# Kernel tuning notes

Hardware: AMD Instinct MI355X
Metric: run time of the kernel (lower is better)

Reference implementation:

```python
import jax, jax.numpy as jnp
import numpy as np

B, L, H = 8, 1024, 1024
E, K, I = 8, 2, 256
N_SHARED = 2
IS = I * N_SHARED
NHEADS = 4
HD = H // NHEADS
EPS = 1e-6


def rmsnorm(x, w):
    xf = x.astype(jnp.float32)
    var = jnp.mean(xf * xf, axis=-1, keepdims=True)
    return w * (xf * jax.lax.rsqrt(var + EPS)).astype(x.dtype)


def setup_inputs():
    key = jax.random.key(0)
    ks = jax.random.split(key, 12)
    s = 0.02
    return {
        "hidden_states": jax.random.normal(ks[0], (B, L, H), jnp.float32),
        "true_counts": jax.random.randint(ks[1], (B,), 1, L + 1),
        "context_norm_w": jnp.ones((H,), jnp.float32),
        "in_proj_w": jax.random.normal(ks[2], (3 * H, H), jnp.float32) * s,
        "in_proj_b": jnp.zeros((3 * H,), jnp.float32),
        "out_proj_w": jax.random.normal(ks[3], (H, H), jnp.float32) * s,
        "out_proj_b": jnp.zeros((H,), jnp.float32),
        "gate_norm_w": jnp.ones((H,), jnp.float32),
        "gate_w": jax.random.normal(ks[4], (E, H), jnp.float32) * s,
        "expert_norm_w": jnp.ones((E, H), jnp.float32),
        "expert_gate_w": jax.random.normal(ks[5], (E, I, H), jnp.float32) * s,
        "expert_up_w": jax.random.normal(ks[6], (E, I, H), jnp.float32) * s,
        "expert_down_w": jax.random.normal(ks[7], (E, H, I), jnp.float32) * s,
        "shared_norm_w": jnp.ones((H,), jnp.float32),
        "shared_gate_w": jax.random.normal(ks[8], (IS, H), jnp.float32) * s,
        "shared_up_w": jax.random.normal(ks[9], (IS, H), jnp.float32) * s,
        "shared_down_w": jax.random.normal(ks[10], (H, IS), jnp.float32) * s,
        "out_gate_w": jnp.zeros((1, H), jnp.float32),
        "out_gate_b": jnp.zeros((1,), jnp.float32),
    }


def reference(hidden_states, true_counts, context_norm_w, in_proj_w, in_proj_b,
              out_proj_w, out_proj_b, gate_norm_w, gate_w, expert_norm_w,
              expert_gate_w, expert_up_w, expert_down_w, shared_norm_w,
              shared_gate_w, shared_up_w, shared_down_w, out_gate_w, out_gate_b):
    Bq, Lq, Hq = hidden_states.shape
    pad = jnp.arange(Lq)[None, :] >= true_counts[:, None]  # [B,L] True = padding

    # --- pre-norm self-attention context layer (eval mode: no dropout) ---
    nx = rmsnorm(hidden_states, context_norm_w)
    qkv = nx @ in_proj_w.T + in_proj_b
    q, k, v = jnp.split(qkv, 3, axis=-1)
    def heads(t):
        return t.reshape(Bq, Lq, NHEADS, HD).transpose(0, 2, 1, 3)
    q, k, v = heads(q), heads(k), heads(v)
    att = jnp.einsum('bhqd,bhkd->bhqk', q, k) / np.float32(np.sqrt(HD))
    att = jnp.where(pad[:, None, None, :], jnp.finfo(att.dtype).min, att)
    att = jax.nn.softmax(att, axis=-1)
    ctx = jnp.einsum('bhqk,bhkd->bhqd', att, v).transpose(0, 2, 1, 3).reshape(Bq, Lq, Hq)
    ctx = ctx @ out_proj_w.T + out_proj_b
    x = hidden_states + ctx
    identity = x

    xf = x.reshape(-1, Hq)  # [N,H]
    N = xf.shape[0]

    # --- top-k gating ---
    gscores = jax.nn.softmax(rmsnorm(xf, gate_norm_w) @ gate_w.T, axis=-1)  # [N,E]
    topw, topi = jax.lax.top_k(gscores, K)
    topw = topw / (jnp.sum(topw, axis=-1, keepdims=True) + 1e-20)  # norm_topk_prob
    w_ne = jnp.zeros((N, E), xf.dtype).at[jnp.arange(N)[:, None], topi].set(topw)

    # --- routed experts: each expert has its own RMSNorm; fold the norm weight
    # into the gate/up projections since rms scale of x is expert-independent ---
    xf32 = xf.astype(jnp.float32)
    xhat = xf * jax.lax.rsqrt(jnp.mean(xf32 * xf32, axis=-1, keepdims=True) + EPS)
    wg = expert_gate_w * expert_norm_w[:, None, :]  # [E,I,H]
    wu = expert_up_w * expert_norm_w[:, None, :]
    g = jax.nn.silu(jnp.einsum('nh,eih->nei', xhat, wg))
    u = jnp.einsum('nh,eih->nei', xhat, wu)
    # weighted combine folded into the down projection (linear in the intermediate)
    y = jnp.einsum('nei,ne,ehi->nh', g * u, w_ne, expert_down_w)
    y = y.reshape(Bq, Lq, Hq)

    # --- shared experts ---
    sx = rmsnorm(identity, shared_norm_w)
    y = y + (jax.nn.silu(sx @ shared_gate_w.T) * (sx @ shared_up_w.T)) @ shared_down_w.T

    # --- output gate + padding mask ---
    gate_score = jax.nn.sigmoid(y @ out_gate_w.T + out_gate_b)  # [B,L,1]
    y_gated = y * gate_score
    y_gated = jnp.where(pad[..., None], jnp.zeros((), y.dtype), y_gated)
    return y_gated
```

## Files before the change

kernel.cpp:

```cpp
#include <hip/hip_runtime.h>
#include <hip/hip_bf16.h>

typedef unsigned short u16;
typedef unsigned int   u32;
typedef short bf16x8 __attribute__((ext_vector_type(8)));
typedef float f32x4  __attribute__((ext_vector_type(4)));

#define DEV static __device__ __forceinline__

#define Bc 8
#define Lc 1024
#define Hc 1024
#define Ec 8
#define Ic 256
#define ISc 512
#define NHc 4
#define HDc 256
#define NTOK 8192
#define EPSc 1e-6f
#define MAXSLOTS 17408

DEV u16 f2bf(float f){
  u32 u = __float_as_uint(f);
  return (u16)((u + 0x7fffu + ((u >> 16) & 1u)) >> 16);
}
DEV float bf2f(u16 h){ return __uint_as_float(((u32)h) << 16); }

DEV void gload_lds16(const void* g, void* l){
  __builtin_amdgcn_global_load_lds((const __attribute__((address_space(1))) u32*)g,
                                   (__attribute__((address_space(3))) u32*)l, 16, 0, 0);
}

DEV bool compact_m0(const int* __restrict__ tc, int slot, int& m0){
  int cb[8], Lt = 0;
#pragma unroll
  for (int b = 0; b < 8; b++){ cb[b] = (tc[b] + 127) >> 7; Lt += cb[b]; }
  const int i = (slot & 7) + 8*(slot >> 3);
  if (i >= Lt) return false;
  int acc = 0, bsel = 0, pos = 0;
#pragma unroll
  for (int b = 0; b < 8; b++){
    if (i < acc + cb[b]){ bsel = b; pos = i - acc; break; }
    acc += cb[b];
  }
  m0 = (bsel*8 + pos)*128;
  return true;
}

template<int EPI, int BIAS, int SKIP, int SWZ, int ZDEC>
__global__ __launch_bounds__(256)
void gemm3(const u16* __restrict__ Ahi, const u16* __restrict__ Alo,
           const u16* __restrict__ Bhi, const u16* __restrict__ Blo,
           void* __restrict__ Cv, const float* __restrict__ bias,
           const float* __restrict__ Res,
           int M, int N, int K, int lda, int ldb, int ldc,
           long sAin, long sAout, long sBin, long sBout, long sCin, long sCout,
           int loOffC, int biasStride, const int* __restrict__ tc, int bbase)
{
  __shared__ u16 lsAh[128*32];
  __shared__ u16 lsAl[128*32];
  __shared__ u16 lsBh[128*32];
  __shared__ u16 lsBl[128*32];
  int m_i, n_i, z;
  if (SWZ == 1){
    const int NB = gridDim.x*gridDim.y;
    const int L = blockIdx.x + gridDim.x*(blockIdx.y + gridDim.y*blockIdx.z);
    const int r = L & 7, k = L >> 3;
    z = r + 8*(k / NB);
    const int idx = k % NB;
    n_i = idx % gridDim.x; m_i = idx / gridDim.x;
  } else if (SWZ == 2){
    m_i = blockIdx.x; n_i = blockIdx.y; z = blockIdx.z;
  } else {
    n_i = blockIdx.x; m_i = blockIdx.y; z = blockIdx.z;
  }
  int n0 = n_i*128, m0 = m_i*128;
  const int zin  = ZDEC ? (z & 7)  : (z & 3);
  const int zout = ZDEC ? (z >> 3) : (z >> 2);
  if (SKIP == 1){ const int c = tc[bbase + zin]; if (m0 >= c || n0 >= c) return; }
  if (SKIP == 2){ const int c = tc[bbase + zin]; if (m0 >= c) return;
                  const int kl = (c + 31) & ~31; K = K < kl ? K : kl; }
  if (SKIP == 3){ if ((m0 & 1023) >= tc[m0 >> 10]) return; }
  if (SKIP == 4){ if (!compact_m0(tc, m_i, m0)) return; }
  const long aoff = (long)zin*sAin + (long)zout*sAout;
  const long boff = (long)zin*sBin + (long)zout*sBout;
  const long coff = (long)zin*sCin + (long)zout*sCout;
  const u16* Ahb = Ahi + aoff;
  const u16* Alb = Alo + aoff;
  const u16* Bhb = Bhi + boff;
  const u16* Blb = Blo + boff;
  const int t = threadIdx.x, lane = t & 63;
  const int w = t >> 6, wm = w >> 1, wn = w & 1;
  const int fr = lane & 15, kg = lane >> 4;
  const int srow = t >> 2, scol = (t & 3) * 8;
  f32x4 acc[4][4] = {};

  for (int kb = 0; kb < K; kb += 32){
    gload_lds16(Ahb + (long)(m0 +      srow)*lda + kb + scol, &lsAh[srow*32 + scol]);
    gload_lds16(Ahb + (long)(m0 + 64 + srow)*lda + kb + scol, &lsAh[(64+srow)*32 + scol]);
    gload_lds16(Alb + (long)(m0 +      srow)*lda + kb + scol, &lsAl[srow*32 + scol]);
    gload_lds16(Alb + (long)(m0 + 64 + srow)*lda + kb + scol, &lsAl[(64+srow)*32 + scol]);
    gload_lds16(Bhb + (long)(n0 +      srow)*ldb + kb + scol, &lsBh[srow*32 + scol]);
    gload_lds16(Bhb + (long)(n0 + 64 + srow)*ldb + kb + scol, &lsBh[(64+srow)*32 + scol]);
    gload_lds16(Blb + (long)(n0 +      srow)*ldb + kb + scol, &lsBl[srow*32 + scol]);
    gload_lds16(Blb + (long)(n0 + 64 + srow)*ldb + kb + scol, &lsBl[(64+srow)*32 + scol]);
    asm volatile("s_waitcnt vmcnt(0)" ::: "memory");
    __syncthreads();
    bf16x8 ah[4], al[4], bh[4], bl[4];
#pragma unroll
    for (int i = 0; i < 4; i++){
      ah[i] = *(const bf16x8*)&lsAh[(wm*64 + i*16 + fr)*32 + kg*8];
      al[i] = *(const bf16x8*)&lsAl[(wm*64 + i*16 + fr)*32 + kg*8];
      bh[i] = *(const bf16x8*)&lsBh[(wn*64 + i*16 + fr)*32 + kg*8];
      bl[i] = *(const bf16x8*)&lsBl[(wn*64 + i*16 + fr)*32 + kg*8];
    }
#pragma unroll
    for (int mi = 0; mi < 4; mi++)
#pragma unroll
      for (int ni = 0; ni < 4; ni++){
        acc[mi][ni] = __builtin_amdgcn_mfma_f32_16x16x32_bf16(ah[mi], bh[ni], acc[mi][ni], 0, 0, 0);
        acc[mi][ni] = __builtin_amdgcn_mfma_f32_16x16x32_bf16(ah[mi], bl[ni], acc[mi][ni], 0, 0, 0);
        acc[mi][ni] = __builtin_amdgcn_mfma_f32_16x16x32_bf16(al[mi], bh[ni], acc[mi][ni], 0, 0, 0);
      }
    __syncthreads();
  }

  const int r4 = (lane >> 4) * 4;
#pragma unroll
  for (int mi = 0; mi < 4; mi++){
#pragma unroll
    for (int ni = 0; ni < 4; ni++){
      const int col = n0 + wn*64 + ni*16 + fr;
      const float bb = BIAS ? bias[zin*biasStride + col] : 0.f;
#pragma unroll
      for (int r = 0; r < 4; r++){
        const int row = m0 + wm*64 + mi*16 + r4 + r;
        float v = acc[mi][ni][r] + bb;
        if (EPI == 0){
          u16 hv = f2bf(v), lv = f2bf(v - bf2f(hv));
          long idx = coff + (long)row*ldc + col;
          ((u16*)Cv)[idx] = hv;
          ((u16*)Cv)[idx + loOffC] = lv;
        } else if (EPI == 1){
          ((float*)Cv)[coff + (long)row*ldc + col] = v;
        } else if (EPI == 2){
          long idx = coff + (long)row*ldc + col;
          ((float*)Cv)[idx] = v + Res[idx];
        } else if (EPI == 3){
          u16 hv = f2bf(v), lv = f2bf(v - bf2f(hv));
          int b = row >> 10, q = row & 1023;
          int h = col >> 8, d = col & 255;
          long o = ((long)(b*NHc + h)*HDc + d)*2048 + q;
          ((u16*)Cv)[o] = hv;
          ((u16*)Cv)[o + 1024] = lv;
        } else {
          u16 hv = f2bf(v), lv = f2bf(v - bf2f(hv));
          if (z < 2){
            long idx = (long)z*sCin + (long)row*ldc + col;
            ((u16*)Cv)[idx] = hv;
            ((u16*)Cv)[idx + loOffC] = lv;
          } else {
            int b = row >> 10, q = row & 1023;
            int h = col >> 8, d = col & 255;
            long o = sCout + ((long)(b*NHc + h)*HDc + d)*2048 + q;
            ((u16*)Cv)[o] = hv;
            ((u16*)Cv)[o + 1024] = lv;
          }
        }
      }
    }
  }
}

template<int EPI, int SKIP, int SWZ>
__global__ __launch_bounds__(256)
void gemm_bt(const u16* __restrict__ A, const u16* __restrict__ B,
             void* __restrict__ Cv,
             int M, int N, int K, int lda, int ldb, int ldc,
             long sAz, long sBz, long sCz, const int* __restrict__ tc)
{
  __shared__ u16 lsA[128*32];
  __shared__ u16 lsB[128*32];
  int m_i, n_i;
  if (SWZ == 2){ m_i = blockIdx.x; n_i = blockIdx.y; }
  else         { n_i = blockIdx.x; m_i = blockIdx.y; }
  const int z = blockIdx.z;
  int n0 = n_i*128, m0 = m_i*128;
  if (SKIP == 3){ if ((m0 & 1023) >= tc[m0 >> 10]) return; }
  if (SKIP == 4){ if (!compact_m0(tc, m_i, m0)) return; }
  const u16* Ab = A + (long)z*sAz;
  const u16* Bb = B + (long)z*sBz;
  const int t = threadIdx.x, lane = t & 63;
  const int w = t >> 6, wm = w >> 1, wn = w & 1;
  const int fr = lane & 15, kg = lane >> 4;
  const int srow = t >> 2, scol = (t & 3) * 8;
  f32x4 acc[4][4] = {};

  for (int kb = 0; kb < K; kb += 32){
    gload_lds16(Ab + (long)(m0 +      srow)*lda + kb + scol, &lsA[srow*32 + scol]);
    gload_lds16(Ab + (long)(m0 + 64 + srow)*lda + kb + scol, &lsA[(64+srow)*32 + scol]);
    gload_lds16(Bb + (long)(n0 +      srow)*ldb + kb + scol, &lsB[srow*32 + scol]);
    gload_lds16(Bb + (long)(n0 + 64 + srow)*ldb + kb + scol, &lsB[(64+srow)*32 + scol]);
    asm volatile("s_waitcnt vmcnt(0)" ::: "memory");
    __syncthreads();
    bf16x8 av[4], bv[4];
#pragma unroll
    for (int i = 0; i < 4; i++){
      av[i] = *(const bf16x8*)&lsA[(wm*64 + i*16 + fr)*32 + kg*8];
      bv[i] = *(const bf16x8*)&lsB[(wn*64 + i*16 + fr)*32 + kg*8];
    }
#pragma unroll
    for (int mi = 0; mi < 4; mi++)
#pragma unroll
      for (int ni = 0; ni < 4; ni++)
        acc[mi][ni] = __builtin_amdgcn_mfma_f32_16x16x32_bf16(av[mi], bv[ni], acc[mi][ni], 0, 0, 0);
    __syncthreads();
  }

  const int r4 = (lane >> 4) * 4;
#pragma unroll
  for (int mi = 0; mi < 4; mi++){
#pragma unroll
    for (int ni = 0; ni < 4; ni++){
      const int col = n0 + wn*64 + ni*16 + fr;
#pragma unroll
      for (int r = 0; r < 4; r++){
        const int row = m0 + wm*64 + mi*16 + r4 + r;
        const long idx = (long)z*sCz + (long)row*ldc + col;
        float v = acc[mi][ni][r];
        if      (EPI == 0) ((u16*)Cv)[idx]   = f2bf(v);
        else if (EPI == 1) ((float*)Cv)[idx] = v;
        else               ((float*)Cv)[idx] += v;
      }
    }
  }
}

__global__ __launch_bounds__(256)
void gemm_gu_gather(const u16* __restrict__ A, const u16* __restrict__ Ball,
                    u16* __restrict__ Cg, const int* __restrict__ sidx,
                    const int* __restrict__ counts, const int* __restrict__ offs)
{
  __shared__ u16 lsA[128*32];
  __shared__ u16 lsB[128*32];
  const int e = blockIdx.z;
  const int cnt = counts[e];
  const int obase = offs[e];
  const int padc = offs[e+1] - obase;
  const int m0 = blockIdx.y*128;
  if (m0 >= padc) return;
  const int n0 = blockIdx.x*128;
  const u16* B = Ball + (long)e*512*1024;
  const int t = threadIdx.x, lane = t & 63;
  const int w = t >> 6, wm = w >> 1, wn = w & 1;
  const int fr = lane & 15, kg = lane >> 4;
  const int srow = t >> 2, scol = (t & 3) * 8;
  const int s0 = m0 + srow, s1 = m0 + 64 + srow;
  const int tok0 = (s0 < cnt) ? sidx[e*NTOK + s0] : 0;
  const int tok1 = (s1 < cnt) ? sidx[e*NTOK + s1] : 0;
  f32x4 acc[4][4] = {};

  for (int kb = 0; kb < 1024; kb += 32){
    gload_lds16(A + (long)tok0*1024 + kb + scol, &lsA[srow*32 + scol]);
    gload_lds16(A + (long)tok1*1024 + kb + scol, &lsA[(64+srow)*32 + scol]);
    gload_lds16(B + (long)(n0 +      srow)*1024 + kb + scol, &lsB[srow*32 + scol]);
    gload_lds16(B + (long)(n0 + 64 + srow)*1024 + kb + scol, &lsB[(64+srow)*32 + scol]);
    asm volatile("s_waitcnt vmcnt(0)" ::: "memory");
    __syncthreads();
    bf16x8 av[4], bv[4];
#pragma unroll
    for (int i = 0; i < 4; i++){
      av[i] = *(const bf16x8*)&lsA[(wm*64 + i*16 + fr)*32 + kg*8];
      bv[i] = *(const bf16x8*)&lsB[(wn*64 + i*16 + fr)*32 + kg*8];
    }
#pragma unroll
    for (int mi = 0; mi < 4; mi++)
#pragma unroll
      for (int ni = 0; ni < 4; ni++)
        acc[mi][ni] = __builtin_amdgcn_mfma_f32_16x16x32_bf16(av[mi], bv[ni], acc[mi][ni], 0, 0, 0);
    __syncthreads();
  }

  const int r4 = (lane >> 4) * 4;
#pragma unroll
  for (int mi = 0; mi < 4; mi++){
#pragma unroll
    for (int ni = 0; ni < 4; ni++){
      const int col = wn*64 + ni*16 + fr + n0;
#pragma unroll
      for (int r = 0; r < 4; r++){
        const int row = m0 + wm*64 + mi*16 + r4 + r;
        Cg[(long)(obase + row)*512 + col] = f2bf(acc[mi][ni][r]);
      }
    }
  }
}

__global__ __launch_bounds__(256)
void gemm_down_slots(const u16* __restrict__ Zg, const u16* __restrict__ Wd,
                     u16* __restrict__ D, const int* __restrict__ offs)
{
  __shared__ u16 lsA[128*32];
  __shared__ u16 lsB[128*32];
  const int m0 = blockIdx.y*128;
  if (m0 >= offs[8]) return;
  int e = 0;
#pragma unroll
  for (int i = 0; i < 7; i++) if (m0 >= offs[i+1]) e = i+1;
  const u16* B = Wd + (long)e*1024*256;
  const int n0 = blockIdx.x*128;
  const int t = threadIdx.x, lane = t & 63;
  const int w = t >> 6, wm = w >> 1, wn = w & 1;
  const int fr = lane & 15, kg = lane >> 4;
  const int srow = t >> 2, scol = (t & 3) * 8;
  f32x4 acc[4][4] = {};

  for (int kb = 0; kb < 256; kb += 32){
    gload_lds16(Zg + (long)(m0 +      srow)*256 + kb + scol, &lsA[srow*32 + scol]);
    gload_lds16(Zg + (long)(m0 + 64 + srow)*256 + kb + scol, &lsA[(64+srow)*32 + scol]);
    gload_lds16(B  + (long)(n0 +      srow)*256 + kb + scol, &lsB[srow*32 + scol]);
    gload_lds16(B  + (long)(n0 + 64 + srow)*256 + kb + scol, &lsB[(64+srow)*32 + scol]);
    asm volatile("s_waitcnt vmcnt(0)" ::: "memory");
    __syncthreads();
    bf16x8 av[4], bv[4];
#pragma unroll
    for (int i = 0; i < 4; i++){
      av[i] = *(const bf16x8*)&lsA[(wm*64 + i*16 + fr)*32 + kg*8];
      bv[i] = *(const bf16x8*)&lsB[(wn*64 + i*16 + fr)*32 + kg*8];
    }
#pragma unroll
    for (int mi = 0; mi < 4; mi++)
#pragma unroll
      for (int ni = 0; ni < 4; ni++)
        acc[mi][ni] = __builtin_amdgcn_mfma_f32_16x16x32_bf16(av[mi], bv[ni], acc[mi][ni], 0, 0, 0);
    __syncthreads();
  }

  const int r4 = (lane >> 4) * 4;
#pragma unroll
  for (int mi = 0; mi < 4; mi++){
#pragma unroll
    for (int ni = 0; ni < 4; ni++){
      const int col = n0 + wn*64 + ni*16 + fr;
#pragma unroll
      for (int r = 0; r < 4; r++){
        const int row = m0 + wm*64 + mi*16 + r4 + r;
        D[(long)row*1024 + col] = f2bf(acc[mi][ni][r]);
      }
    }
  }
}

__global__ void cast_bf16_k(const float* __restrict__ in, u16* __restrict__ out, long n){
  long i = (long)blockIdx.x*blockDim.x + threadIdx.x;
  long st = (long)gridDim.x*blockDim.x;
  for (; i < n; i += st) out[i] = f2bf(in[i]);
}

__global__ void split_cast_k(const float* __restrict__ in, u16* __restrict__ hi,
                             u16* __restrict__ lo, long n){
  long i = (long)blockIdx.x*blockDim.x + threadIdx.x;
  long st = (long)gridDim.x*blockDim.x;
  for (; i < n; i += st){
    float v = in[i];
    u16 h = f2bf(v);
    hi[i] = h;
    lo[i] = f2bf(v - bf2f(h));
  }
}

__global__ void fold_expert_k(const float* __restrict__ g, const float* __restrict__ u,
                              const float* __restrict__ nw, u16* __restrict__ gu, long n){
  long i = (long)blockIdx.x*blockDim.x + threadIdx.x;
  long st = (long)gridDim.x*blockDim.x;
  for (; i < n; i += st){
    int h  = (int)(i & (Hc - 1));
    int ii = (int)((i >> 10) & (Ic - 1));
    int e  = (int)(i >> 18);
    float wv = nw[e*Hc + h];
    long o = (long)e*(2*Ic*Hc) + (long)ii*Hc + h;
    gu[o]         = f2bf(g[i]*wv);
    gu[o + Ic*Hc] = f2bf(u[i]*wv);
  }
}

__global__ __launch_bounds__(256)
void rmsnorm_split_k(const float* __restrict__ x, const float* __restrict__ w1,
                     u16* __restrict__ o){
  const int row = blockIdx.x, t = threadIdx.x, lane = t & 63, w = t >> 6;
  float4 v = ((const float4*)(x + (long)row*Hc))[t];
  float ss = v.x*v.x + v.y*v.y + v.z*v.z + v.w*v.w;
  for (int off = 32; off; off >>= 1) ss += __shfl_xor(ss, off);
  __shared__ float red[4];
  if (lane == 0) red[w] = ss;
  __syncthreads();
  float rs = rsqrtf((red[0]+red[1]+red[2]+red[3])*(1.f/Hc) + EPSc);
  float4 wv = ((const float4*)w1)[t];
  float f0 = v.x*rs*wv.x, f1 = v.y*rs*wv.y, f2 = v.z*rs*wv.z, f3 = v.w*rs*wv.w;
  ushort4 hv, lv;
  hv.x = f2bf(f0); lv.x = f2bf(f0 - bf2f(hv.x));
  hv.y = f2bf(f1); lv.y = f2bf(f1 - bf2f(hv.y));
  hv.z = f2bf(f2); lv.z = f2bf(f2 - bf2f(hv.z));
  hv.w = f2bf(f3); lv.w = f2bf(f3 - bf2f(hv.w));
  u16* r16 = o + (long)row*2048;
  ((ushort4*)r16)[t] = hv;
  ((ushort4*)(r16 + 1024))[t] = lv;
}

__global__ __launch_bounds__(256)
void norm_gate_k(const float* __restrict__ x, const float* __restrict__ shw,
                 const float* __restrict__ gnw, const float* __restrict__ gw,
                 const int* __restrict__ tcnt,
                 u16* __restrict__ xhat, u16* __restrict__ sx,
                 int* __restrict__ topi, float* __restrict__ topw){
  const int row = blockIdx.x, t = threadIdx.x, lane = t & 63, w = t >> 6;
  float4 v = ((const float4*)(x + (long)row*Hc))[t];
  float ss = v.x*v.x + v.y*v.y + v.z*v.z + v.w*v.w;
  for (int off = 32; off; off >>= 1) ss += __shfl_xor(ss, off);
  __shared__ float red[4];
  __shared__ float gred[4][8];
  if (lane == 0) red[w] = ss;
  __syncthreads();
  float rs = rsqrtf((red[0]+red[1]+red[2]+red[3])*(1.f/Hc) + EPSc);
  ushort4 ov;
  ov.x = f2bf(v.x*rs); ov.y = f2bf(v.y*rs); ov.z = f2bf(v.z*rs); ov.w = f2bf(v.w*rs);
  ((ushort4*)xhat)[(long)row*256 + t] = ov;
  float4 sv = ((const float4*)shw)[t];
  ov.x = f2bf(v.x*rs*sv.x); ov.y = f2bf(v.y*rs*sv.y);
  ov.z = f2bf(v.z*rs*sv.z); ov.w = f2bf(v.w*rs*sv.w);
  ((ushort4*)sx)[(long)row*256 + t] = ov;

  const int b = row >> 10, l = row & 1023;
  if (l >= tcnt[b]) return;
  float4 g = ((const float4*)gnw)[t];
  float xg0 = v.x*g.x, xg1 = v.y*g.y, xg2 = v.z*g.z, xg3 = v.w*g.w;
  float pe[8];
#pragma unroll
  for (int e = 0; e < 8; e++){
    float4 ww = ((const float4*)(gw + (long)e*Hc))[t];
    pe[e] = xg0*ww.x + xg1*ww.y + xg2*ww.z + xg3*ww.w;
  }
  for (int off = 32; off; off >>= 1){
#pragma unroll
    for (int e = 0; e < 8; e++) pe[e] += __shfl_xor(pe[e], off);
  }
  if (lane == 0){
#pragma unroll
    for (int e = 0; e < 8; e++) gred[w][e] = pe[e];
  }
  __syncthreads();
  if (t == 0){
    float sc[8], m = -3.4e38f;
#pragma unroll
    for (int e = 0; e < 8; e++){
      sc[e] = (gred[0][e]+gred[1][e]+gred[2][e]+gred[3][e])*rs;
      m = fmaxf(m, sc[e]);
    }
    float p[8], sum = 0.f;
#pragma unroll
    for (int e = 0; e < 8; e++){ p[e] = __expf(sc[e] - m); sum += p[e]; }
    float inv = 1.f/sum;
#pragma unroll
    for (int e = 0; e < 8; e++) p[e] *= inv;
    int i1 = 0; float v1 = p[0];
#pragma unroll
    for (int e = 1; e < 8; e++) if (p[e] > v1){ v1 = p[e]; i1 = e; }
    int i2 = -1; float v2 = -1.f;
#pragma unroll
    for (int e = 0; e < 8; e++) if (e != i1 && p[e] > v2){ v2 = p[e]; i2 = e; }
    float dn = v1 + v2 + 1e-20f;
    topi[2*row] = i1; topi[2*row + 1] = i2;
    topw[2*row] = v1/dn; topw[2*row + 1] = v2/dn;
  }
}

__global__ __launch_bounds__(256)
void softmax2_k(float* __restrict__ S, const int* __restrict__ cnt, int bbase, int bmask){
  const int rid = blockIdx.x;
  const int b = bbase + ((rid >> 10) & bmask);
  const int n = cnt[b];
  if ((rid & 1023) >= n) return;
  float* row = S + (long)rid*Lc;
  const int t = threadIdx.x, lane = t & 63, w = t >> 6;
  float4 v = ((const float4*)row)[t];
  const float sc = 0.0625f;
  float vals[4] = {v.x*sc, v.y*sc, v.z*sc, v.w*sc};
  const int c = t*4;
  float m = -3.4e38f;
#pragma unroll
  for (int j = 0; j < 4; j++) if (c + j < n) m = fmaxf(m, vals[j]);
  for (int o = 32; o; o >>= 1) m = fmaxf(m, __shfl_xor(m, o));
  __shared__ float red[8];
  if (lane == 0) red[w] = m;
  __syncthreads();
  m = fmaxf(fmaxf(red[0], red[1]), fmaxf(red[2], red[3]));
  float p[4], s = 0.f;
#pragma unroll
  for (int j = 0; j < 4; j++){ p[j] = (c + j < n) ? __expf(vals[j] - m) : 0.f; s += p[j]; }
  for (int o = 32; o; o >>= 1) s += __shfl_xor(s, o);
  if (lane == 0) red[4 + w] = s;
  __syncthreads();
  const float inv = 1.f / (red[4]+red[5]+red[6]+red[7]);
  ushort4 hv, lv;
  float q0 = p[0]*inv, q1 = p[1]*inv, q2 = p[2]*inv, q3 = p[3]*inv;
  hv.x = f2bf(q0); lv.x = f2bf(q0 - bf2f(hv.x));
  hv.y = f2bf(q1); lv.y = f2bf(q1 - bf2f(hv.y));
  hv.z = f2bf(q2); lv.z = f2bf(q2 - bf2f(hv.z));
  hv.w = f2bf(q3); lv.w = f2bf(q3 - bf2f(hv.w));
  u16* r16 = (u16*)S + (long)rid*2048;
  ((ushort4*)r16)[t] = hv;
  ((ushort4*)(r16 + 1024))[t] = lv;
}

__global__ __launch_bounds__(1024)
void route_scan_k(const int* __restrict__ tcnt, const int* __restrict__ topi,
                  const float* __restrict__ topw, int* __restrict__ counts,
                  int* __restrict__ offs, int* __restrict__ sidx,
                  int* __restrict__ gpos, float* __restrict__ wG){
  __shared__ int hist[1024][8];
  __shared__ int soffs[9];
  const int t = threadIdx.x;
  for (int i = t; i < MAXSLOTS; i += 1024) wG[i] = 0.f;
  int h[8] = {0,0,0,0,0,0,0,0};
  const int n0 = t*8;
  int e0[8], e1[8];
#pragma unroll
  for (int k = 0; k < 8; k++){
    const int n = n0 + k;
    const int b = n >> 10, l = n & 1023;
    const bool val = l < tcnt[b];
    e0[k] = val ? topi[2*n]   : -1;
    e1[k] = val ? topi[2*n+1] : -1;
    if (val){ h[e0[k]]++; h[e1[k]]++; }
  }
#pragma unroll
  for (int e = 0; e < 8; e++) hist[t][e] = h[e];
  __syncthreads();
  for (int off = 1; off < 1024; off <<= 1){
    int v[8];
#pragma unroll
    for (int e = 0; e < 8; e++)
      v[e] = hist[t][e] + ((t >= off) ? hist[t - off][e] : 0);
    __syncthreads();
#pragma unroll
    for (int e = 0; e < 8; e++) hist[t][e] = v[e];
    __syncthreads();
  }
  if (t == 0){
    int o = 0; soffs[0] = 0; offs[0] = 0;
    for (int e = 0; e < 8; e++){
      int c = hist[1023][e];
      counts[e] = c;
      o += (c + 127) & ~127;
      soffs[e+1] = o;
      offs[e+1] = o;
    }
  }
  __syncthreads();
  int run[8];
#pragma unroll
  for (int e = 0; e < 8; e++) run[e] = hist[t][e] - h[e];
#pragma unroll
  for (int k = 0; k < 8; k++){
    const int n = n0 + k;
    if (e0[k] >= 0){
      const int p0 = run[e0[k]]++;
      const int p1 = run[e1[k]]++;
      sidx[e0[k]*NTOK + p0] = n;
      sidx[e1[k]*NTOK + p1] = n;
      const int g0 = soffs[e0[k]] + p0, g1 = soffs[e1[k]] + p1;
      gpos[2*n] = g0; gpos[2*n+1] = g1;
      wG[g0] = topw[2*n]; wG[g1] = topw[2*n+1];
    } else {
      gpos[2*n] = 0; gpos[2*n+1] = 0;
    }
  }
}

__global__ void act_shared_k(const u16* __restrict__ gu, u16* __restrict__ z, long n){
  long i = (long)blockIdx.x*blockDim.x + threadIdx.x;
  long st = (long)gridDim.x*blockDim.x;
  for (; i < n; i += st){
    long nn = i >> 9;
    int  ii = (int)(i & (ISc - 1));
    float gv = bf2f(gu[nn*1024 + ii]);
    float uv = bf2f(gu[nn*1024 + ISc + ii]);
    z[i] = f2bf(gv/(1.f + __expf(-gv)) * uv);
  }
}

__global__ void act_slots_k(const u16* __restrict__ gu, const float* __restrict__ wG,
                            const int* __restrict__ offs, u16* __restrict__ z){
  long nmax = (long)offs[8]*256;
  long st = (long)gridDim.x*blockDim.x;
  for (long i = (long)blockIdx.x*blockDim.x + threadIdx.x; i < nmax; i += st){
    long s = i >> 8;
    int ii = (int)(i & 255);
    float gv = bf2f(gu[s*512 + ii]);
    float uv = bf2f(gu[s*512 + 256 + ii]);
    z[i] = f2bf(gv/(1.f + __expf(-gv)) * uv * wG[s]);
  }
}

__global__ void act_expert_k(const u16* __restrict__ gu, const int* __restrict__ topi,
                             const float* __restrict__ topw, int e,
                             u16* __restrict__ z, long n){
  long i = (long)blockIdx.x*blockDim.x + threadIdx.x;
  long st = (long)gridDim.x*blockDim.x;
  for (; i < n; i += st){
    long nn = i >> 8;
    int  ii = (int)(i & (Ic - 1));
    float wv = 0.f;
    if      (topi[2*nn]     == e) wv = topw[2*nn];
    else if (topi[2*nn + 1] == e) wv = topw[2*nn + 1];
    float gv = bf2f(gu[nn*512 + ii]);
    float uv = bf2f(gu[nn*512 + Ic + ii]);
    z[i] = f2bf(gv/(1.f + __expf(-gv)) * uv * wv);
  }
}

__global__ __launch_bounds__(256)
void final2_k(const float* __restrict__ ysh, const u16* __restrict__ D,
              const int* __restrict__ gpos, const float* __restrict__ ogw,
              const float* __restrict__ ogb, const int* __restrict__ cnt,
              float* __restrict__ out){
  const int t = threadIdx.x, lane = t & 63, w = t >> 6;
  const int n = blockIdx.x*4 + w;
  const int b = n >> 10, l = n & 1023;
  float* outr = out + (long)n*Hc;
  if (l >= cnt[b]){
#pragma unroll
    for (int j = 0; j < 16; j++) outr[j*64 + lane] = 0.f;
    return;
  }
  const float* yr = ysh + (long)n*Hc;
  const u16* d0 = D + (long)gpos[2*n]*1024;
  const u16* d1 = D + (long)gpos[2*n+1]*1024;
  float dot = 0.f, yv[16];
#pragma unroll
  for (int j = 0; j < 16; j++){
    int d = j*64 + lane;
    yv[j] = yr[d] + bf2f(d0[d]) + bf2f(d1[d]);
    dot += yv[j]*ogw[d];
  }
  for (int o = 32; o; o >>= 1) dot += __shfl_xor(dot, o);
  float s = 1.f/(1.f + __expf(-(dot + ogb[0])));
#pragma unroll
  for (int j = 0; j < 16; j++) outr[j*64 + lane] = yv[j]*s;
}

__global__ __launch_bounds__(256)
void final_k(const float* __restrict__ y, const float* __restrict__ ogw,
             const float* __restrict__ ogb, const int* __restrict__ cnt,
             float* __restrict__ out){
  const int t = threadIdx.x, lane = t & 63, w = t >> 6;
  const int n = blockIdx.x*4 + w;
  const int b = n >> 10, l = n & 1023;
  const bool pad = l >= cnt[b];
  const float* yr = y + (long)n*Hc;
  float dot = 0.f, yv[16];
#pragma unroll
  for (int j = 0; j < 16; j++){
    int d = j*64 + lane;
    yv[j] = yr[d];
    dot += yv[j]*ogw[d];
  }
  for (int o = 32; o; o >>= 1) dot += __shfl_xor(dot, o);
  float s = 1.f/(1.f + __expf(-(dot + ogb[0])));
  float* outr = out + (long)n*Hc;
#pragma unroll
  for (int j = 0; j < 16; j++){
    int d = j*64 + lane;
    outr[d] = pad ? 0.f : yv[j]*s;
  }
}

__global__ void sentinel_k(float* out){ out[0] = 1.0e9f; }

extern "C" void kernel_launch(void* const* d_in, const int* in_sizes, int n_in,
                              void* d_out, int out_size, void* d_ws, size_t ws_size,
                              hipStream_t stream){
  const float* hidden  = (const float*)d_in[0];
  const int*   cnt     = (const int*)  d_in[1];
  const float* ctx_nw  = (const float*)d_in[2];
  const float* Wqkv    = (const float*)d_in[3];
  const float* in_b    = (const float*)d_in[4];
  const float* Woutp   = (const float*)d_in[5];
  const float* out_b   = (const float*)d_in[6];
  const float* gate_nw = (const float*)d_in[7];
  const float* gate_w  = (const float*)d_in[8];
  const float* exp_nw  = (const float*)d_in[9];
  const float* Weg     = (const float*)d_in[10];
  const float* Weu     = (const float*)d_in[11];
  const float* Wed     = (const float*)d_in[12];
  const float* sh_nw   = (const float*)d_in[13];
  const float* Wsg     = (const float*)d_in[14];
  const float* Wsu     = (const float*)d_in[15];
  const float* Wsd     = (const float*)d_in[16];
  const float* ogw     = (const float*)d_in[17];
  const float* ogb     = (const float*)d_in[18];
  float* out = (float*)d_out;

  const size_t MB = 1024*1024;
  char* ws = (char*)d_ws;
  size_t off = 0;
  auto alloc = [&](size_t bytes)->char*{
    char* p = ws + off; off += (bytes + 255) & ~(size_t)255; return p;
  };
  u16* wWqH  = (u16*)alloc((size_t)3072*1024*2);
  u16* wWqL  = (u16*)alloc((size_t)3072*1024*2);
  u16* wWoH  = (u16*)alloc((size_t)1024*1024*2);
  u16* wWoL  = (u16*)alloc((size_t)1024*1024*2);
  u16* wWgu  = (u16*)alloc((size_t)Ec*2*Ic*Hc*2);
  u16* wWd   = (u16*)alloc((size_t)Ec*Hc*Ic*2);
  u16* wWsgu = (u16*)alloc((size_t)2*ISc*Hc*2);
  u16* wWsd  = (u16*)alloc((size_t)Hc*ISc*2);
  int*   wTopI = (int*)  alloc((size_t)NTOK*2*4);
  float* wTopW = (float*)alloc((size_t)NTOK*2*4);
  int*   wGpos = (int*)  alloc((size_t)NTOK*2*4);
  int*   wSidx = (int*)  alloc((size_t)Ec*NTOK*4);
  float* wG    = (float*)alloc((size_t)MAXSLOTS*4);
  int*   wCnts = (int*)  alloc(64);
  int*   wOffs = (int*)  alloc(64);
  char* P1 = alloc(32*MB);
  char* P2 = alloc(32*MB);
  char* P3 = alloc(32*MB);
  char* P4 = alloc(32*MB);
  size_t fixed = off;
  const int mode = (fixed + 128*MB <= ws_size) ? 2 :
                   (fixed + 64*MB  <= ws_size) ? 1 : 0;
  char* P5 = alloc(mode == 2 ? 128*MB : mode == 1 ? 64*MB : 16*MB);
  if (off > ws_size){ sentinel_k<<<1,1,0,stream>>>(out); return; }

  u16*   wNx   = (u16*)P1;
  u16*   wCtx  = (u16*)P1;
  float* wY    = (float*)P1;
  u16*   wQp   = (u16*)P2;
  u16*   wXhat = (u16*)P2;
  u16*   wSx   = (u16*)(P2 + 16*MB);
  u16*   wKp   = (u16*)P3;
  float* wX    = (float*)P3;
  u16*   wGUg  = (u16*)P3;
  u16*   wZg   = (u16*)(P3 + 18*MB);
  u16*   wGUe  = (u16*)P3;
  u16*   wZe   = (u16*)(P3 + 8*MB);
  u16*   wVtp  = (u16*)P4;
  u16*   wGUs  = (u16*)P4;
  u16*   wZs   = (u16*)(P4 + 16*MB);
  float* wS    = (float*)P5;
  u16*   wD    = (u16*)P5;

  split_cast_k<<<4096, 256, 0, stream>>>(Wqkv,  wWqH, wWqL, (long)3072*1024);
  split_cast_k<<<2048, 256, 0, stream>>>(Woutp, wWoH, wWoL, (long)1024*1024);
  cast_bf16_k<<<2048, 256, 0, stream>>>(Wed, wWd, (long)Ec*Hc*Ic);
  cast_bf16_k<<<1024, 256, 0, stream>>>(Wsg, wWsgu,                (long)ISc*Hc);
  cast_bf16_k<<<1024, 256, 0, stream>>>(Wsu, wWsgu + (long)ISc*Hc, (long)ISc*Hc);
  cast_bf16_k<<<1024, 256, 0, stream>>>(Wsd, wWsd, (long)Hc*ISc);
  fold_expert_k<<<2048, 256, 0, stream>>>(Weg, Weu, exp_nw, wWgu, (long)Ec*Ic*Hc);

  rmsnorm_split_k<<<NTOK, 256, 0, stream>>>(hidden, ctx_nw, wNx);
  gemm3<4, 1, 4, 2, 0><<<dim3(64, 8, 3), 256, 0, stream>>>(
      wNx, wNx + 1024, wWqH, wWqL, wQp, in_b, nullptr,
      NTOK, 1024, 1024, 2048, 1024, 2048,
      0, 0, (long)1024*1024, 0,
      (long)16*1024*1024,
      (long)32*1024*1024,
      1024, 1024, cnt, 0);

  if (mode == 2){
    gemm3<1, 0, 1, 1, 1><<<dim3(8, 8, 32), 256, 0, stream>>>(
        wQp, wQp + 1024, wKp, wKp + 1024, wS, nullptr, nullptr,
        Lc, Lc, HDc, 2048, 2048, Lc,
        (long)Lc*2048, (long)HDc,
        (long)Lc*2048, (long)HDc,
        (long)Lc*Lc,   (long)8*Lc*Lc,
        0, 0, cnt, 0);
    softmax2_k<<<32*1024, 256, 0, stream>>>(wS, cnt, 0, 7);
    gemm3<0, 0, 2, 1, 1><<<dim3(2, 8, 32), 256, 0, stream>>>(
        (const u16*)wS, (const u16*)wS + 1024, wVtp, wVtp + 1024, wCtx,
        nullptr, nullptr,
        Lc, HDc, Lc, 2048, 2048, 2048,
        (long)Lc*2048,      (long)8*Lc*2048,
        (long)NHc*HDc*2048, (long)HDc*2048,
        (long)Lc*2048,      (long)HDc,
        1024, 0, cnt, 0);
  } else if (mode == 1){
    for (int g = 0; g < 2; g++){
      const int bbase = g*4;
      const long tokoff = (long)g*4*Lc*2048;
      const u16* Qb = wQp + tokoff;
      const u16* Kb = wKp + tokoff;
      gemm3<1, 0, 1, 1, 0><<<dim3(8, 8, 16), 256, 0, stream>>>(
          Qb, Qb + 1024, Kb, Kb + 1024, wS, nullptr, nullptr,
          Lc, Lc, HDc, 2048, 2048, Lc,
          (long)Lc*2048, (long)HDc,
          (long)Lc*2048, (long)HDc,
          (long)Lc*Lc,   (long)4*Lc*Lc,
          0, 0, cnt, bbase);
      softmax2_k<<<16*1024, 256, 0, stream>>>(wS, cnt, bbase, 3);
      const u16* Vb = wVtp + (long)g*4*NHc*HDc*2048;
      u16* Cb = wCtx + tokoff;
      gemm3<0, 0, 2, 1, 0><<<dim3(2, 8, 16), 256, 0, stream>>>(
          (const u16*)wS, (const u16*)wS + 1024, Vb, Vb + 1024, Cb, nullptr, nullptr,
          Lc, HDc, Lc, 2048, 2048, 2048,
          (long)Lc*2048,     (long)4*Lc*2048,
          (long)NHc*HDc*2048,(long)HDc*2048,
          (long)Lc*2048,     (long)HDc,
          1024, 0, cnt, bbase);
    }
  } else {
    for (int g = 0; g < 8; g++){
      const int hf = g >> 2, hbase = g & 3, bbase = hf*4;
      const long tokoff = (long)hf*4*Lc*2048;
      const u16* Qb = wQp + tokoff + hbase*HDc;
      const u16* Kb = wKp + tokoff + hbase*HDc;
      gemm3<1, 0, 1, 0, 0><<<dim3(8, 8, 4), 256, 0, stream>>>(
          Qb, Qb + 1024, Kb, Kb + 1024, wS, nullptr, nullptr,
          Lc, Lc, HDc, 2048, 2048, Lc,
          (long)Lc*2048, (long)HDc,
          (long)Lc*2048, (long)HDc,
          (long)Lc*Lc,   (long)4*Lc*Lc,
          0, 0, cnt, bbase);
      softmax2_k<<<4*1024, 256, 0, stream>>>(wS, cnt, bbase, 3);
      const u16* Vb = wVtp + (long)hf*4*NHc*HDc*2048 + (long)hbase*HDc*2048;
      u16* Cb = wCtx + tokoff + hbase*HDc;
      gemm3<0, 0, 2, 0, 0><<<dim3(2, 8, 4), 256, 0, stream>>>(
          (const u16*)wS, (const u16*)wS + 1024, Vb, Vb + 1024, Cb, nullptr, nullptr,
          Lc, HDc, Lc, 2048, 2048, 2048,
          (long)Lc*2048,     (long)4*Lc*2048,
          (long)NHc*HDc*2048,(long)HDc*2048,
          (long)Lc*2048,     (long)HDc,
          1024, 0, cnt, bbase);
    }
  }

  gemm3<2, 1, 4, 2, 0><<<dim3(64, 8, 1), 256, 0, stream>>>(
      wCtx, wCtx + 1024, wWoH, wWoL, wX, out_b, hidden,
      NTOK, 1024, 1024, 2048, 1024, 1024,
      0, 0, 0, 0, 0, 0, 0, 0, cnt, 0);

  norm_gate_k<<<NTOK, 256, 0, stream>>>(wX, sh_nw, gate_nw, gate_w, cnt,
                                        wXhat, wSx, wTopI, wTopW);
  route_scan_k<<<1, 1024, 0, stream>>>(cnt, wTopI, wTopW, wCnts, wOffs,
                                       wSidx, wGpos, wG);

  gemm_bt<0, 4, 2><<<dim3(64, 8, 1), 256, 0, stream>>>(
      wSx, wWsgu, wGUs, NTOK, 2*ISc, 1024, 1024, 1024, 2*ISc, 0, 0, 0, cnt);
  act_shared_k<<<4096, 256, 0, stream>>>(wGUs, wZs, (long)NTOK*ISc);
  gemm_bt<1, 4, 2><<<dim3(64, 8, 1), 256, 0, stream>>>(
      wZs, wWsd, wY, NTOK, 1024, ISc, ISc, ISc, 1024, 0, 0, 0, cnt);

  if (mode >= 1){
    gemm_gu_gather<<<dim3(4, 64, Ec), 256, 0, stream>>>(
        wXhat, wWgu, wGUg, wSidx, wCnts, wOffs);
    act_slots_k<<<2048, 256, 0, stream>>>(wGUg, wG, wOffs, wZg);
    gemm_down_slots<<<dim3(8, MAXSLOTS/128, 1), 256, 0, stream>>>(
        wZg, wWd, wD, wOffs);
    final2_k<<<NTOK/4, 256, 0, stream>>>(wY, wD, wGpos, ogw, ogb, cnt, out);
  } else {
    for (int e = 0; e < Ec; e++){
      gemm_bt<0, 0, 0><<<dim3(4, 64, 1), 256, 0, stream>>>(
          wXhat, wWgu + (long)e*2*Ic*Hc, wGUe, NTOK, 2*Ic, 1024, 1024, 1024, 2*Ic,
          0, 0, 0, nullptr);
      act_expert_k<<<2048, 256, 0, stream>>>(wGUe, wTopI, wTopW, e, wZe, (long)NTOK*Ic);
      gemm_bt<2, 0, 0><<<dim3(8, 64, 1), 256, 0, stream>>>(
          wZe, wWd + (long)e*Hc*Ic, wY, NTOK, 1024, Ic, Ic, Ic, 1024, 0, 0, 0, nullptr);
    }
    final_k<<<NTOK/4, 256, 0, stream>>>(wY, ogw, ogb, cnt, out);
  }
}
```

Baseline: 661.9 us.

## Double-buffer LDS tiles in all MFMA GEMM kernels to overlap loads with compute

Converts the four GEMM kernels (split-precision gemm3, gemm_bt, the gathered expert gate/up GEMM, and the slot-based down GEMM) to use two LDS buffers. Each iteration prefetches the next K-tile while MFMAs run on the current one, hiding global-load latency behind compute. This doubles LDS use per block, to 64 KB for gemm3, which can lower occupancy. It also drops the explicit s_waitcnt vmcnt(0) before the barrier, so correctness relies on __syncthreads waiting for the direct-to-LDS loads to finish.

```diff
diff --git a/kernel.cpp b/kernel.cpp
--- a/kernel.cpp
+++ b/kernel.cpp
@@ -57,10 +57,10 @@
            long sAin, long sAout, long sBin, long sBout, long sCin, long sCout,
            int loOffC, int biasStride, const int* __restrict__ tc, int bbase)
 {
-  __shared__ u16 lsAh[128*32];
-  __shared__ u16 lsAl[128*32];
-  __shared__ u16 lsBh[128*32];
-  __shared__ u16 lsBl[128*32];
+  __shared__ u16 lsAh[2][128*32];
+  __shared__ u16 lsAl[2][128*32];
+  __shared__ u16 lsBh[2][128*32];
+  __shared__ u16 lsBl[2][128*32];
   int m_i, n_i, z;
   if (SWZ == 1){
     const int NB = gridDim.x*gridDim.y;
@@ -95,24 +95,29 @@
   const int srow = t >> 2, scol = (t & 3) * 8;
   f32x4 acc[4][4] = {};
 
+  auto stage = [&](int buf, int kb){
+    gload_lds16(Ahb + (long)(m0 +      srow)*lda + kb + scol, &lsAh[buf][srow*32 + scol]);
+    gload_lds16(Ahb + (long)(m0 + 64 + srow)*lda + kb + scol, &lsAh[buf][(64+srow)*32 + scol]);
+    gload_lds16(Alb + (long)(m0 +      srow)*lda + kb + scol, &lsAl[buf][srow*32 + scol]);
+    gload_lds16(Alb + (long)(m0 + 64 + srow)*lda + kb + scol, &lsAl[buf][(64+srow)*32 + scol]);
+    gload_lds16(Bhb + (long)(n0 +      srow)*ldb + kb + scol, &lsBh[buf][srow*32 + scol]);
+    gload_lds16(Bhb + (long)(n0 + 64 + srow)*ldb + kb + scol, &lsBh[buf][(64+srow)*32 + scol]);
+    gload_lds16(Blb + (long)(n0 +      srow)*ldb + kb + scol, &lsBl[buf][srow*32 + scol]);
+    gload_lds16(Blb + (long)(n0 + 64 + srow)*ldb + kb + scol, &lsBl[buf][(64+srow)*32 + scol]);
+  };
+
+  stage(0, 0);
+  __syncthreads();
+  int cur = 0;
   for (int kb = 0; kb < K; kb += 32){
-    gload_lds16(Ahb + (long)(m0 +      srow)*lda + kb + scol, &lsAh[srow*32 + scol]);
-    gload_lds16(Ahb + (long)(m0 + 64 + srow)*lda + kb + scol, &lsAh[(64+srow)*32 + scol]);
-    gload_lds16(Alb + (long)(m0 +      srow)*lda + kb + scol, &lsAl[srow*32 + scol]);
-    gload_lds16(Alb + (long)(m0 + 64 + srow)*lda + kb + scol, &lsAl[(64+srow)*32 + scol]);
-    gload_lds16(Bhb + (long)(n0 +      srow)*ldb + kb + scol, &lsBh[srow*32 + scol]);
-    gload_lds16(Bhb + (long)(n0 + 64 + srow)*ldb + kb + scol, &lsBh[(64+srow)*32 + scol]);
-    gload_lds16(Blb + (long)(n0 +      srow)*ldb + kb + scol, &lsBl[srow*32 + scol]);
-    gload_lds16(Blb + (long)(n0 + 64 + srow)*ldb + kb + scol, &lsBl[(64+srow)*32 + scol]);
-    asm volatile("s_waitcnt vmcnt(0)" ::: "memory");
-    __syncthreads();
+    if (kb + 32 < K) stage(cur ^ 1, kb + 32);
     bf16x8 ah[4], al[4], bh[4], bl[4];
 #pragma unroll
     for (int i = 0; i < 4; i++){
-      ah[i] = *(const bf16x8*)&lsAh[(wm*64 + i*16 + fr)*32 + kg*8];
-      al[i] = *(const bf16x8*)&lsAl[(wm*64 + i*16 + fr)*32 + kg*8];
-      bh[i] = *(const bf16x8*)&lsBh[(wn*64 + i*16 + fr)*32 + kg*8];
-      bl[i] = *(const bf16x8*)&lsBl[(wn*64 + i*16 + fr)*32 + kg*8];
+      ah[i] = *(const bf16x8*)&lsAh[cur][(wm*64 + i*16 + fr)*32 + kg*8];
+      al[i] = *(const bf16x8*)&lsAl[cur][(wm*64 + i*16 + fr)*32 + kg*8];
+      bh[i] = *(const bf16x8*)&lsBh[cur][(wn*64 + i*16 + fr)*32 + kg*8];
+      bl[i] = *(const bf16x8*)&lsBl[cur][(wn*64 + i*16 + fr)*32 + kg*8];
     }
 #pragma unroll
     for (int mi = 0; mi < 4; mi++)
@@ -123,6 +128,7 @@
         acc[mi][ni] = __builtin_amdgcn_mfma_f32_16x16x32_bf16(al[mi], bh[ni], acc[mi][ni], 0, 0, 0);
       }
     __syncthreads();
+    cur ^= 1;
   }
 
   const int r4 = (lane >> 4) * 4;
@@ -179,8 +185,8 @@
              int M, int N, int K, int lda, int ldb, int ldc,
              long sAz, long sBz, long sCz, const int* __restrict__ tc)
 {
-  __shared__ u16 lsA[128*32];
-  __shared__ u16 lsB[128*32];
+  __shared__ u16 lsA[2][128*32];
+  __shared__ u16 lsB[2][128*32];
   int m_i, n_i;
   if (SWZ == 2){ m_i = blockIdx.x; n_i = blockIdx.y; }
   else         { n_i = blockIdx.x; m_i = blockIdx.y; }
@@ -196,18 +202,23 @@
   const int srow = t >> 2, scol = (t & 3) * 8;
   f32x4 acc[4][4] = {};
 
+  auto stage = [&](int buf, int kb){
+    gload_lds16(Ab + (long)(m0 +      srow)*lda + kb + scol, &lsA[buf][srow*32 + scol]);
+    gload_lds16(Ab + (long)(m0 + 64 + srow)*lda + kb + scol, &lsA[buf][(64+srow)*32 + scol]);
+    gload_lds16(Bb + (long)(n0 +      srow)*ldb + kb + scol, &lsB[buf][srow*32 + scol]);
+    gload_lds16(Bb + (long)(n0 + 64 + srow)*ldb + kb + scol, &lsB[buf][(64+srow)*32 + scol]);
+  };
+
+  stage(0, 0);
+  __syncthreads();
+  int cur = 0;
   for (int kb = 0; kb < K; kb += 32){
-    gload_lds16(Ab + (long)(m0 +      srow)*lda + kb + scol, &lsA[srow*32 + scol]);
-    gload_lds16(Ab + (long)(m0 + 64 + srow)*lda + kb + scol, &lsA[(64+srow)*32 + scol]);
-    gload_lds16(Bb + (long)(n0 +      srow)*ldb + kb + scol, &lsB[srow*32 + scol]);
-    gload_lds16(Bb + (long)(n0 + 64 + srow)*ldb + kb + scol, &lsB[(64+srow)*32 + scol]);
-    asm volatile("s_waitcnt vmcnt(0)" ::: "memory");
-    __syncthreads();
+    if (kb + 32 < K) stage(cur ^ 1, kb + 32);
     bf16x8 av[4], bv[4];
 #pragma unroll
     for (int i = 0; i < 4; i++){
-      av[i] = *(const bf16x8*)&lsA[(wm*64 + i*16 + fr)*32 + kg*8];
-      bv[i] = *(const bf16x8*)&lsB[(wn*64 + i*16 + fr)*32 + kg*8];
+      av[i] = *(const bf16x8*)&lsA[cur][(wm*64 + i*16 + fr)*32 + kg*8];
+      bv[i] = *(const bf16x8*)&lsB[cur][(wn*64 + i*16 + fr)*32 + kg*8];
     }
 #pragma unroll
     for (int mi = 0; mi < 4; mi++)
@@ -215,6 +226,7 @@
       for (int ni = 0; ni < 4; ni++)
         acc[mi][ni] = __builtin_amdgcn_mfma_f32_16x16x32_bf16(av[mi], bv[ni], acc[mi][ni], 0, 0, 0);
     __syncthreads();
+    cur ^= 1;
   }
 
   const int r4 = (lane >> 4) * 4;
@@ -241,8 +253,8 @@
                     u16* __restrict__ Cg, const int* __restrict__ sidx,
                     const int* __restrict__ counts, const int* __restrict__ offs)
 {
-  __shared__ u16 lsA[128*32];
-  __shared__ u16 lsB[128*32];
+  __shared__ u16 lsA[2][128*32];
+  __shared__ u16 lsB[2][128*32];
   const int e = blockIdx.z;
   const int cnt = counts[e];
   const int obase = offs[e];
@@ -260,18 +272,23 @@
   const int tok1 = (s1 < cnt) ? sidx[e*NTOK + s1] : 0;
   f32x4 acc[4][4] = {};
 
+  auto stage = [&](int buf, int kb){
+    gload_lds16(A + (long)tok0*1024 + kb + scol, &lsA[buf][srow*32 + scol]);
+    gload_lds16(A + (long)tok1*1024 + kb + scol, &lsA[buf][(64+srow)*32 + scol]);
+    gload_lds16(B + (long)(n0 +      srow)*1024 + kb + scol, &lsB[buf][srow*32 + scol]);
+    gload_lds16(B + (long)(n0 + 64 + srow)*1024 + kb + scol, &lsB[buf][(64+srow)*32 + scol]);
+  };
+
+  stage(0, 0);
+  __syncthreads();
+  int cur = 0;
   for (int kb = 0; kb < 1024; kb += 32){
-    gload_lds16(A + (long)tok0*1024 + kb + scol, &lsA[srow*32 + scol]);
-    gload_lds16(A + (long)tok1*1024 + kb + scol, &lsA[(64+srow)*32 + scol]);
-    gload_lds16(B + (long)(n0 +      srow)*1024 + kb + scol, &lsB[srow*32 + scol]);
-    gload_lds16(B + (long)(n0 + 64 + srow)*1024 + kb + scol, &lsB[(64+srow)*32 + scol]);
-    asm volatile("s_waitcnt vmcnt(0)" ::: "memory");
-    __syncthreads();
+    if (kb + 32 < 1024) stage(cur ^ 1, kb + 32);
     bf16x8 av[4], bv[4];
 #pragma unroll
     for (int i = 0; i < 4; i++){
-      av[i] = *(const bf16x8*)&lsA[(wm*64 + i*16 + fr)*32 + kg*8];
-      bv[i] = *(const bf16x8*)&lsB[(wn*64 + i*16 + fr)*32 + kg*8];
+      av[i] = *(const bf16x8*)&lsA[cur][(wm*64 + i*16 + fr)*32 + kg*8];
+      bv[i] = *(const bf16x8*)&lsB[cur][(wn*64 + i*16 + fr)*32 + kg*8];
     }
 #pragma unroll
     for (int mi = 0; mi < 4; mi++)
@@ -279,6 +296,7 @@
       for (int ni = 0; ni < 4; ni++)
         acc[mi][ni] = __builtin_amdgcn_mfma_f32_16x16x32_bf16(av[mi], bv[ni], acc[mi][ni], 0, 0, 0);
     __syncthreads();
+    cur ^= 1;
   }
 
   const int r4 = (lane >> 4) * 4;
@@ -300,8 +318,8 @@
 void gemm_down_slots(const u16* __restrict__ Zg, const u16* __restrict__ Wd,
                      u16* __restrict__ D, const int* __restrict__ offs)
 {
-  __shared__ u16 lsA[128*32];
-  __shared__ u16 lsB[128*32];
+  __shared__ u16 lsA[2][128*32];
+  __shared__ u16 lsB[2][128*32];
   const int m0 = blockIdx.y*128;
   if (m0 >= offs[8]) return;
   int e = 0;
@@ -315,18 +333,23 @@
   const int srow = t >> 2, scol = (t & 3) * 8;
   f32x4 acc[4][4] = {};
 
+  auto stage = [&](int buf, int kb){
+    gload_lds16(Zg + (long)(m0 +      srow)*256 + kb + scol, &lsA[buf][srow*32 + scol]);
+    gload_lds16(Zg + (long)(m0 + 64 + srow)*256 + kb + scol, &lsA[buf][(64+srow)*32 + scol]);
+    gload_lds16(B  + (long)(n0 +      srow)*256 + kb + scol, &lsB[buf][srow*32 + scol]);
+    gload_lds16(B  + (long)(n0 + 64 + srow)*256 + kb + scol, &lsB[buf][(64+srow)*32 + scol]);
+  };
+
+  stage(0, 0);
+  __syncthreads();
+  int cur = 0;
   for (int kb = 0; kb < 256; kb += 32){
-    gload_lds16(Zg + (long)(m0 +      srow)*256 + kb + scol, &lsA[srow*32 + scol]);
-    gload_lds16(Zg + (long)(m0 + 64 + srow)*256 + kb + scol, &lsA[(64+srow)*32 + scol]);
-    gload_lds16(B  + (long)(n0 +      srow)*256 + kb + scol, &lsB[srow*32 + scol]);
-    gload_lds16(B  + (long)(n0 + 64 + srow)*256 + kb + scol, &lsB[(64+srow)*32 + scol]);
-    asm volatile("s_waitcnt vmcnt(0)" ::: "memory");
-    __syncthreads();
+    if (kb + 32 < 256) stage(cur ^ 1, kb + 32);
     bf16x8 av[4], bv[4];
 #pragma unroll
     for (int i = 0; i < 4; i++){
-      av[i] = *(const bf16x8*)&lsA[(wm*64 + i*16 + fr)*32 + kg*8];
-      bv[i] = *(const bf16x8*)&lsB[(wn*64 + i*16 + fr)*32 + kg*8];
+      av[i] = *(const bf16x8*)&lsA[cur][(wm*64 + i*16 + fr)*32 + kg*8];
+      bv[i] = *(const bf16x8*)&lsB[cur][(wn*64 + i*16 + fr)*32 + kg*8];
     }
 #pragma unroll
     for (int mi = 0; mi < 4; mi++)
@@ -334,6 +357,7 @@
       for (int ni = 0; ni < 4; ni++)
         acc[mi][ni] = __builtin_amdgcn_mfma_f32_16x16x32_bf16(av[mi], bv[ni], acc[mi][ni], 0, 0, 0);
     __syncthreads();
+    cur ^= 1;
   }
 
   const int r4 = (lane >> 4) * 4;
```

After: 610.0 us. -7.8%, faster.
